# Optimization experiments

Measured on AMD Instinct MI355X. Metric: run time of the kernel, lower is better.

## Reference

```python
import jax, jax.numpy as jnp
import numpy as np
from jax import lax

B, T, H, F, K, NB, MAXLEN = 32, 1024, 384, 384, 3, 256, 2048


def _ln(x, g, b, eps=1e-5):
    m = jnp.mean(x, axis=-1, keepdims=True)
    v = jnp.var(x, axis=-1, keepdims=True)
    return (x - m) * lax.rsqrt(v + eps) * g + b


def _conv(x, w, b):
    # x: (B, T, Cin), w: (K, Cin, Cout); SAME padding == torch padding=(K-1)//2 for K=3, stride 1
    y = lax.conv_general_dilated(x, w, (1,), 'SAME', dimension_numbers=('NWC', 'WIO', 'NWC'))
    return y + b


def _predictor(x, mask, w1, b1, g1, be1, w2, b2, g2, be2, wo, bo):
    h = _ln(jax.nn.relu(_conv(x, w1, b1)), g1, be1)
    h = _ln(jax.nn.relu(_conv(h, w2, b2)), g2, be2)
    out = jnp.einsum('btf,f->bt', h, wo) + bo  # Linear(F -> 1).squeeze(-1)
    return jnp.where(mask, 0.0, out)


def _length_regulate(x, dur, max_len):
    # vectorized equivalent of torch per-sample expand+cat+pad
    csum = jnp.cumsum(dur, axis=1)                      # (B, T)
    total = csum[:, -1]                                 # (B,) = mel_len
    frames = jnp.arange(max_len)                        # (M,)
    # frame f belongs to phoneme i with csum[i-1] <= f < csum[i]
    idx = jax.vmap(lambda c: jnp.searchsorted(c, frames, side='right'))(csum)  # (B, M)
    idx = jnp.clip(idx, 0, x.shape[1] - 1)
    out = jnp.take_along_axis(x, idx[:, :, None], axis=1)                      # (B, M, H)
    valid = (frames[None, :] < total[:, None]).astype(x.dtype)                 # zero-pad tail
    return out * valid[:, :, None], total


def setup_inputs() -> dict:
    key = jax.random.key(0)
    ks = iter(jax.random.split(key, 64))
    nk = lambda: next(ks)
    d = {}
    d['x'] = jax.random.normal(nk(), (B, T, H), jnp.float32)
    d['src_mask'] = jnp.zeros((B, T), jnp.bool_)
    d['duration'] = jax.random.randint(nk(), (B, T), 0, 4)
    d['max_len'] = MAXLEN
    for p in ('dp', 'pp', 'ep'):
        d[p + '_w1'] = jax.random.normal(nk(), (K, H, F), jnp.float32) * 0.02
        d[p + '_b1'] = jnp.zeros((F,), jnp.float32)
        d[p + '_g1'] = jnp.ones((F,), jnp.float32)
        d[p + '_be1'] = jnp.zeros((F,), jnp.float32)
        d[p + '_w2'] = jax.random.normal(nk(), (K, F, F), jnp.float32) * 0.02
        d[p + '_b2'] = jnp.zeros((F,), jnp.float32)
        d[p + '_g2'] = jnp.ones((F,), jnp.float32)
        d[p + '_be2'] = jnp.zeros((F,), jnp.float32)
        d[p + '_wo'] = jax.random.normal(nk(), (F,), jnp.float32) * 0.02
        d[p + '_bo'] = jnp.zeros((1,), jnp.float32)
    d['pitch_bins'] = jnp.linspace(0.0, 1.0, NB - 1, dtype=jnp.float32)
    d['energy_bins'] = jnp.linspace(0.0, 1.0, NB - 1, dtype=jnp.float32)
    d['pitch_emb'] = jax.random.normal(nk(), (NB, H), jnp.float32) * 0.02
    d['energy_emb'] = jax.random.normal(nk(), (NB, H), jnp.float32) * 0.02
    d['pitch_target'] = jax.random.uniform(nk(), (B, T), jnp.float32)
    d['energy_target'] = jax.random.uniform(nk(), (B, T), jnp.float32)
    return d


def reference(x, src_mask, duration, max_len,
              dp_w1, dp_b1, dp_g1, dp_be1, dp_w2, dp_b2, dp_g2, dp_be2, dp_wo, dp_bo,
              pp_w1, pp_b1, pp_g1, pp_be1, pp_w2, pp_b2, pp_g2, pp_be2, pp_wo, pp_bo,
              ep_w1, ep_b1, ep_g1, ep_be1, ep_w2, ep_b2, ep_g2, ep_be2, ep_wo, ep_bo,
              pitch_bins, energy_bins, pitch_emb, energy_emb, pitch_target, energy_target):
    log_dur = _predictor(x, src_mask, dp_w1, dp_b1, dp_g1, dp_be1, dp_w2, dp_b2, dp_g2, dp_be2, dp_wo, dp_bo)
    # phoneme-level pitch (target path: bucketize target, torch.bucketize right=False == searchsorted left)
    pitch_pred = _predictor(x, src_mask, pp_w1, pp_b1, pp_g1, pp_be1, pp_w2, pp_b2, pp_g2, pp_be2, pp_wo, pp_bo)
    x = x + pitch_emb[jnp.searchsorted(pitch_bins, pitch_target, side='left')]
    # phoneme-level energy (predictor sees x AFTER pitch embedding add, as in torch)
    energy_pred = _predictor(x, src_mask, ep_w1, ep_b1, ep_g1, ep_be1, ep_w2, ep_b2, ep_g2, ep_be2, ep_wo, ep_bo)
    x = x + energy_emb[jnp.searchsorted(energy_bins, energy_target, side='left')]
    x_out, mel_len = _length_regulate(x, duration, max_len)
    return (x_out, pitch_pred, energy_pred, log_dur, mel_len)
```

## Files before the change

### kernel.cpp

```cpp
#include <hip/hip_runtime.h>

#define B_ 32
#define T_ 1024
#define C_ 384
#define MAXLEN_ 2048
#define NBINS_ 255
#define WPK1 442368
#define ARS 392
#define TROWS 62
#define NTILE 17

typedef __attribute__((ext_vector_type(8))) short short8v;
typedef __attribute__((ext_vector_type(4))) float floatx4;

__device__ __forceinline__ unsigned short f2bf(float f) {
    unsigned u = __float_as_uint(f);
    u += 0x7fffu + ((u >> 16) & 1u);
    return (unsigned short)(u >> 16);
}

__device__ __forceinline__ const unsigned short* rfl(const unsigned short* p) {
    unsigned long long u = (unsigned long long)p;
    unsigned lo = __builtin_amdgcn_readfirstlane((unsigned)u);
    unsigned hi = __builtin_amdgcn_readfirstlane((unsigned)(u >> 32));
    return (const unsigned short*)(((unsigned long long)hi << 32) | lo);
}

struct CvP {
    const float* xf;
    const unsigned short* wpk;
    const float* b1[3];  const float* g1[3];  const float* be1[3];
    const float* b2[3];  const float* g2[3];  const float* be2[3];
    const float* wo[3];  const float* bo[3];
    float* pred[3];
    const float* pbins; const float* pemb; const float* ptgt;
};

__global__ __launch_bounds__(512, 4) void conv_fused3(CvP P)
{
    __shared__ unsigned short As[66 * ARS];
    __shared__ float redS[8 * 64];
    __shared__ float redQ[8 * 64];
    __shared__ float prbuf[512];
    __shared__ int embi[66];

    const int tid  = threadIdx.x;
    const int wave = tid >> 6;
    const int lane = tid & 63;
    const int lq   = lane >> 4;
    const int ln   = lane & 15;
    const int blk  = blockIdx.x;
    const int p    = blk / (B_ * NTILE);
    const int rem  = blk - p * (B_ * NTILE);
    const int b    = rem / NTILE;
    const int k    = rem - b * NTILE;
    const int t0   = k * TROWS;
    const int nb   = wave * 48;

    const unsigned short* b1s = rfl(P.wpk + (size_t)p * WPK1 + wave * 1536);
    const int lo8 = lane * 8;
    short8v bA[3], bB[3];
#pragma unroll
    for (int nt = 0; nt < 3; ++nt) {
        bA[nt] = *(const short8v*)(b1s + lo8 + (nt << 9));
        bB[nt] = *(const short8v*)(b1s + lo8 + 12288 + (nt << 9));
    }

    const bool fuse_emb = (p == 2);
    if (fuse_emb) {
        if (tid < 66) {
            const int t = t0 - 2 + tid;
            int lo = 0;
            if ((unsigned)t < (unsigned)T_) {
                const float tg = P.ptgt[(b << 10) + t];
                int hi = NBINS_;
                while (lo < hi) {
                    const int mid = (lo + hi) >> 1;
                    if (P.pbins[mid] < tg) lo = mid + 1; else hi = mid;
                }
            }
            embi[tid] = lo;
        }
        __syncthreads();
    }
    for (int i = tid; i < 66 * 96; i += 512) {
        const int row = i / 96;
        const int c4  = i - row * 96;
        const int t   = t0 - 2 + row;
        uint2 pv = make_uint2(0u, 0u);
        if ((unsigned)t < (unsigned)T_) {
            float4 f = *(const float4*)(P.xf + ((size_t)(b << 10) + t) * C_ + c4 * 4);
            if (fuse_emb) {
                const float* er = P.pemb + (size_t)embi[row] * C_ + c4 * 4;
                f.x += er[0]; f.y += er[1]; f.z += er[2]; f.w += er[3];
            }
            asm("v_cvt_pk_bf16_f32 %0, %1, %2" : "=v"(pv.x) : "v"(f.x), "v"(f.y));
            asm("v_cvt_pk_bf16_f32 %0, %1, %2" : "=v"(pv.y) : "v"(f.z), "v"(f.w));
        }
        *(uint2*)&As[row * ARS + c4 * 4] = pv;
    }
    __syncthreads();

    floatx4 acc[12];
#pragma unroll
    for (int i = 0; i < 12; ++i) acc[i] = (floatx4){0.f, 0.f, 0.f, 0.f};

    const unsigned short* abase = &As[ln * ARS + lq * 8];

    {
        int offA = lo8 + 2 * 12288;
        int offB = lo8 + 3 * 12288;
#pragma unroll
        for (int kc = 0; kc < 3; ++kc) {
#pragma unroll
            for (int h2 = 0; h2 < 6; ++h2) {
                const int hb = h2 * 64;
                const int r  = kc * 12 + h2 * 2;
                {
                    short8v afrag[4];
#pragma unroll
                    for (int mt = 0; mt < 4; ++mt)
                        afrag[mt] = *(const short8v*)(abase + (mt * 16 + kc) * ARS + hb);
#pragma unroll
                    for (int mt = 0; mt < 4; ++mt)
#pragma unroll
                        for (int nt = 0; nt < 3; ++nt)
                            acc[mt * 3 + nt] = __builtin_amdgcn_mfma_f32_16x16x32_bf16(
                                afrag[mt], bA[nt], acc[mt * 3 + nt], 0, 0, 0);
                    if (r + 2 < 36) {
#pragma unroll
                        for (int nt = 0; nt < 3; ++nt)
                            bA[nt] = *(const short8v*)(b1s + offA + (nt << 9));
                        offA += 24576;
                    }
                }
                {
                    short8v afrag[4];
#pragma unroll
                    for (int mt = 0; mt < 4; ++mt)
                        afrag[mt] = *(const short8v*)(abase + (mt * 16 + kc) * ARS + hb + 32);
#pragma unroll
                    for (int mt = 0; mt < 4; ++mt)
#pragma unroll
                        for (int nt = 0; nt < 3; ++nt)
                            acc[mt * 3 + nt] = __builtin_amdgcn_mfma_f32_16x16x32_bf16(
                                afrag[mt], bB[nt], acc[mt * 3 + nt], 0, 0, 0);
                    if (r + 3 < 36) {
#pragma unroll
                        for (int nt = 0; nt < 3; ++nt)
                            bB[nt] = *(const short8v*)(b1s + offB + (nt << 9));
                        offB += 24576;
                    }
                }
            }
        }
    }
    __syncthreads();

    float c1b[3], c1g[3], c1be[3];
#pragma unroll
    for (int nt = 0; nt < 3; ++nt) {
        const int col = nb + nt * 16 + ln;
        c1b[nt]  = P.b1[p][col];
        c1g[nt]  = P.g1[p][col];
        c1be[nt] = P.be1[p][col];
    }
#pragma unroll
    for (int mt = 0; mt < 4; ++mt) {
#pragma unroll
        for (int rg = 0; rg < 4; ++rg) {
            float s = 0.f, q = 0.f;
#pragma unroll
            for (int nt = 0; nt < 3; ++nt) {
                float v = acc[mt * 3 + nt][rg] + c1b[nt];
                v = v > 0.f ? v : 0.f;
                acc[mt * 3 + nt][rg] = v;
                s += v; q += v * v;
            }
#pragma unroll
            for (int off = 1; off < 16; off <<= 1) {
                s += __shfl_xor(s, off, 64);
                q += __shfl_xor(q, off, 64);
            }
            if (ln == ((mt * 4 + rg) & 15)) {
                redS[wave * 64 + mt * 16 + lq * 4 + rg] = s;
                redQ[wave * 64 + mt * 16 + lq * 4 + rg] = q;
            }
        }
    }
    __syncthreads();

#pragma unroll
    for (int mt = 0; mt < 4; ++mt) {
#pragma unroll
        for (int rg = 0; rg < 4; ++rg) {
            const int j  = mt * 16 + lq * 4 + rg;
            const int th = t0 - 1 + j;
            float s = 0.f, q = 0.f;
#pragma unroll
            for (int w = 0; w < 8; ++w) {
                s += redS[w * 64 + j];
                q += redQ[w * 64 + j];
            }
            const float m  = s * (1.f / 384.f);
            const float rs = rsqrtf(q * (1.f / 384.f) - m * m + 1e-5f);
            const bool valid = (unsigned)th < (unsigned)T_;
#pragma unroll
            for (int nt = 0; nt < 3; ++nt) {
                float v = (acc[mt * 3 + nt][rg] - m) * rs * c1g[nt] + c1be[nt];
                if (!valid) v = 0.f;
                As[j * ARS + nb + nt * 16 + ln] = f2bf(v);
            }
        }
    }

    const unsigned short* b2s = rfl(P.wpk + (size_t)(3 + p) * WPK1 + wave * 1536);
#pragma unroll
    for (int nt = 0; nt < 3; ++nt) {
        bA[nt] = *(const short8v*)(b2s + lo8 + (nt << 9));
        bB[nt] = *(const short8v*)(b2s + lo8 + 12288 + (nt << 9));
    }
    __syncthreads();

#pragma unroll
    for (int i = 0; i < 12; ++i) acc[i] = (floatx4){0.f, 0.f, 0.f, 0.f};

    {
        int offA = lo8 + 2 * 12288;
        int offB = lo8 + 3 * 12288;
#pragma unroll
        for (int kc = 0; kc < 3; ++kc) {
#pragma unroll
            for (int h2 = 0; h2 < 6; ++h2) {
                const int hb = h2 * 64;
                const int r  = kc * 12 + h2 * 2;
                {
                    short8v afrag[4];
#pragma unroll
                    for (int mt = 0; mt < 4; ++mt)
                        afrag[mt] = *(const short8v*)(abase + (mt * 16 + kc) * ARS + hb);
#pragma unroll
                    for (int mt = 0; mt < 4; ++mt)
#pragma unroll
                        for (int nt = 0; nt < 3; ++nt)
                            acc[mt * 3 + nt] = __builtin_amdgcn_mfma_f32_16x16x32_bf16(
                                afrag[mt], bA[nt], acc[mt * 3 + nt], 0, 0, 0);
                    if (r + 2 < 36) {
#pragma unroll
                        for (int nt = 0; nt < 3; ++nt)
                            bA[nt] = *(const short8v*)(b2s + offA + (nt << 9));
                        offA += 24576;
                    }
                }
                {
                    short8v afrag[4];
#pragma unroll
                    for (int mt = 0; mt < 4; ++mt)
                        afrag[mt] = *(const short8v*)(abase + (mt * 16 + kc) * ARS + hb + 32);
#pragma unroll
                    for (int mt = 0; mt < 4; ++mt)
#pragma unroll
                        for (int nt = 0; nt < 3; ++nt)
                            acc[mt * 3 + nt] = __builtin_amdgcn_mfma_f32_16x16x32_bf16(
                                afrag[mt], bB[nt], acc[mt * 3 + nt], 0, 0, 0);
                    if (r + 3 < 36) {
#pragma unroll
                        for (int nt = 0; nt < 3; ++nt)
                            bB[nt] = *(const short8v*)(b2s + offB + (nt << 9));
                        offB += 24576;
                    }
                }
            }
        }
    }

    float c2b[3], c2g[3], c2be[3], cwo[3];
#pragma unroll
    for (int nt = 0; nt < 3; ++nt) {
        const int col = nb + nt * 16 + ln;
        c2b[nt]  = P.b2[p][col];
        c2g[nt]  = P.g2[p][col];
        c2be[nt] = P.be2[p][col];
        cwo[nt]  = P.wo[p][col];
    }
#pragma unroll
    for (int mt = 0; mt < 4; ++mt) {
#pragma unroll
        for (int rg = 0; rg < 4; ++rg) {
            float s = 0.f, q = 0.f;
#pragma unroll
            for (int nt = 0; nt < 3; ++nt) {
                float v = acc[mt * 3 + nt][rg] + c2b[nt];
                v = v > 0.f ? v : 0.f;
                acc[mt * 3 + nt][rg] = v;
                s += v; q += v * v;
            }
#pragma unroll
            for (int off = 1; off < 16; off <<= 1) {
                s += __shfl_xor(s, off, 64);
                q += __shfl_xor(q, off, 64);
            }
            if (ln == ((mt * 4 + rg) & 15)) {
                redS[wave * 64 + mt * 16 + lq * 4 + rg] = s;
                redQ[wave * 64 + mt * 16 + lq * 4 + rg] = q;
            }
        }
    }
    __syncthreads();

#pragma unroll
    for (int mt = 0; mt < 4; ++mt) {
#pragma unroll
        for (int rg = 0; rg < 4; ++rg) {
            const int row = mt * 16 + lq * 4 + rg;
            float s = 0.f, q = 0.f;
#pragma unroll
            for (int w = 0; w < 8; ++w) {
                s += redS[w * 64 + row];
                q += redQ[w * 64 + row];
            }
            const float m  = s * (1.f / 384.f);
            const float rs = rsqrtf(q * (1.f / 384.f) - m * m + 1e-5f);
            float pr = 0.f;
#pragma unroll
            for (int nt = 0; nt < 3; ++nt)
                pr += ((acc[mt * 3 + nt][rg] - m) * rs * c2g[nt] + c2be[nt]) * cwo[nt];
#pragma unroll
            for (int off = 1; off < 16; off <<= 1)
                pr += __shfl_xor(pr, off, 64);
            if (ln == ((mt * 4 + rg) & 15))
                prbuf[wave * 64 + row] = pr;
        }
    }
    __syncthreads();
    if (tid < 64) {
        const int t = t0 + tid;
        if (tid < TROWS && t < T_) {
            float s = P.bo[p][0];
#pragma unroll
            for (int w = 0; w < 8; ++w) s += prbuf[w * 64 + tid];
            P.pred[p][(b << 10) + t] = s;
        }
    }
}

#define WSS 388
__global__ __launch_bounds__(256) void pack_w_kernel(
    const float* __restrict__ s0, const float* __restrict__ s1,
    const float* __restrict__ s2, const float* __restrict__ s3,
    const float* __restrict__ s4, const float* __restrict__ s5,
    unsigned short* __restrict__ dst)
{
    __shared__ float ws[32 * WSS];
    const int blk  = blockIdx.x;
    const int wsel = blk / 36;
    const int r    = blk - wsel * 36;
    const float* src = wsel == 0 ? s0 : wsel == 1 ? s1 : wsel == 2 ? s2
                     : wsel == 3 ? s3 : wsel == 4 ? s4 : s5;
    const int tid = threadIdx.x;

    const float* sb = src + (size_t)r * 32 * C_;
    for (int i4 = tid; i4 < 3072; i4 += 256) {
        const int k  = i4 / 96;
        const int n4 = i4 - k * 96;
        *(float4*)&ws[k * WSS + n4 * 4] = *(const float4*)(sb + (size_t)k * C_ + n4 * 4);
    }
    __syncthreads();

    unsigned short* db = dst + (size_t)wsel * WPK1 + (size_t)r * 12288;
    for (int c = tid; c < 1536; c += 256) {
        const int lane = c & 63;
        const int wnt  = c >> 6;
        const int ln   = lane & 15;
        const int lq   = lane >> 4;
        const int n    = wnt * 16 + ln;
        ushort4 o0, o1;
        unsigned short e[8];
#pragma unroll
        for (int j = 0; j < 8; ++j)
            e[j] = f2bf(ws[(lq * 8 + j) * WSS + n]);
        o0 = make_ushort4(e[0], e[1], e[2], e[3]);
        o1 = make_ushort4(e[4], e[5], e[6], e[7]);
        *(ushort4*)(db + wnt * 512 + lane * 8)     = o0;
        *(ushort4*)(db + wnt * 512 + lane * 8 + 4) = o1;
    }
}

__global__ __launch_bounds__(256) void cumsum_idx_kernel(
    const int* __restrict__ dur,
    const float* __restrict__ pbins, const float* __restrict__ ptgt,
    const float* __restrict__ ebins, const float* __restrict__ etgt,
    int* __restrict__ xidx, float* __restrict__ mel_len)
{
    __shared__ int cs[T_];
    __shared__ int part[256];
    __shared__ float pb[NBINS_], eb[NBINS_];
    const int b = blockIdx.x;
    const int tid = threadIdx.x;
    if (tid < NBINS_) { pb[tid] = pbins[tid]; eb[tid] = ebins[tid]; }
    int l[4];
    int s = 0;
#pragma unroll
    for (int i = 0; i < 4; ++i) { l[i] = dur[(b << 10) + tid * 4 + i]; s += l[i]; }
    part[tid] = s;
    __syncthreads();
    for (int off = 1; off < 256; off <<= 1) {
        int u = 0;
        if (tid >= off) u = part[tid - off];
        __syncthreads();
        part[tid] += u;
        __syncthreads();
    }
    const int incl = part[tid];
    int run = incl - s;
#pragma unroll
    for (int i = 0; i < 4; ++i) {
        run += l[i];
        cs[tid * 4 + i] = run;
    }
    if (tid == 255) mel_len[b] = (float)incl;
    __syncthreads();
    const int total = cs[T_ - 1];
    for (int f = tid; f < MAXLEN_; f += 256) {
        int pk = -1;
        if (f < total) {
            int lo = 0, hi = T_;
            while (lo < hi) {
                const int mid = (lo + hi) >> 1;
                if (cs[mid] <= f) lo = mid + 1; else hi = mid;
            }
            const int t = lo > T_ - 1 ? T_ - 1 : lo;
            const int row = (b << 10) + t;
            const float ptg = ptgt[row];
            int plo = 0, phi = NBINS_;
            while (plo < phi) {
                const int mid = (plo + phi) >> 1;
                if (pb[mid] < ptg) plo = mid + 1; else phi = mid;
            }
            const float etg = etgt[row];
            int elo = 0, ehi = NBINS_;
            while (elo < ehi) {
                const int mid = (elo + ehi) >> 1;
                if (eb[mid] < etg) elo = mid + 1; else ehi = mid;
            }
            pk = t | (plo << 10) | (elo << 19);
        }
        xidx[(b << 11) + f] = pk;
    }
}

__global__ __launch_bounds__(256) void length_reg_kernel(
    const float* __restrict__ x, const int* __restrict__ xidx,
    const float* __restrict__ pemb, const float* __restrict__ eemb,
    float* __restrict__ out)
{
    const int g    = blockIdx.x * 256 + threadIdx.x;
    const int c4   = g % 96;
    const int rest = g / 96;
    const int frame = rest & (MAXLEN_ - 1);
    const int b     = rest >> 11;
    const int pk = xidx[(b << 11) + frame];
    float4 v = make_float4(0.f, 0.f, 0.f, 0.f);
    if (pk >= 0) {
        const int t   = pk & 1023;
        const int plo = (pk >> 10) & 511;
        const int elo = (pk >> 19) & 511;
        v = *(const float4*)(x + ((size_t)(b << 10) + t) * C_ + c4 * 4);
        const float4 pe = *(const float4*)(pemb + (size_t)plo * C_ + c4 * 4);
        const float4 ee = *(const float4*)(eemb + (size_t)elo * C_ + c4 * 4);
        v.x += pe.x + ee.x; v.y += pe.y + ee.y;
        v.z += pe.z + ee.z; v.w += pe.w + ee.w;
    }
    *(float4*)(out + (size_t)g * 4) = v;
}

extern "C" void kernel_launch(void* const* d_in, const int* in_sizes, int n_in,
                              void* d_out, int out_size, void* d_ws, size_t ws_size,
                              hipStream_t stream)
{
    const float* x        = (const float*)d_in[0];
    const int*   duration = (const int*)d_in[2];
    const float* P[3][10];
    for (int p = 0; p < 3; ++p)
        for (int q = 0; q < 10; ++q)
            P[p][q] = (const float*)d_in[4 + p * 10 + q];
    const float* pitch_bins    = (const float*)d_in[34];
    const float* energy_bins   = (const float*)d_in[35];
    const float* pitch_emb     = (const float*)d_in[36];
    const float* energy_emb    = (const float*)d_in[37];
    const float* pitch_target  = (const float*)d_in[38];
    const float* energy_target = (const float*)d_in[39];

    float* out_x      = (float*)d_out;
    float* out_pitch  = out_x + (size_t)B_ * MAXLEN_ * C_;
    float* out_energy = out_pitch + B_ * T_;
    float* out_logdur = out_energy + B_ * T_;
    float* out_mellen = out_logdur + B_ * T_;

    unsigned short* wpk = (unsigned short*)d_ws;
    int* xidx = (int*)(wpk + (size_t)6 * WPK1);

    const dim3 blk(256);
    const dim3 cblk(512);

    pack_w_kernel<<<216, blk, 0, stream>>>(
        P[0][0], P[0][4], P[1][0], P[1][4], P[2][0], P[2][4], wpk);

    CvP Pa;
    Pa.xf = x; Pa.wpk = wpk;
    for (int p = 0; p < 3; ++p) {
        Pa.b1[p]  = P[p][1];
        Pa.g1[p]  = P[p][2];
        Pa.be1[p] = P[p][3];
        Pa.b2[p]  = P[p][5];
        Pa.g2[p]  = P[p][6];
        Pa.be2[p] = P[p][7];
        Pa.wo[p]  = P[p][8];
        Pa.bo[p]  = P[p][9];
    }
    Pa.pred[0] = out_logdur; Pa.pred[1] = out_pitch; Pa.pred[2] = out_energy;
    Pa.pbins = pitch_bins; Pa.pemb = pitch_emb; Pa.ptgt = pitch_target;

    conv_fused3<<<3 * B_ * NTILE, cblk, 0, stream>>>(Pa);

    cumsum_idx_kernel<<<B_, blk, 0, stream>>>(
        duration, pitch_bins, pitch_target, energy_bins, energy_target,
        xidx, out_mellen);
    length_reg_kernel<<<24576, blk, 0, stream>>>(
        x, xidx, pitch_emb, energy_emb, out_x);
}
```

Before: 490.7 us.

## Add MFMA priority hints, centralize LayerNorm stats, restructure staging loop

Wraps each MFMA burst in s_setprio(1)/s_setprio(0) so waves issuing matrix ops get scheduling priority over waves doing loads. LayerNorm mean and rsqrt are now computed once per row by 64 threads into shared arrays, instead of every thread redundantly summing 8 partials per row. The input staging loop drops the per-iteration division for incremental row/column stepping. Gamma and beta loads are deferred to shorten register live ranges, at the cost of an extra barrier per LayerNorm.

```diff
diff --git a/kernel.cpp b/kernel.cpp
--- a/kernel.cpp
+++ b/kernel.cpp
@@ -42,6 +42,7 @@
     __shared__ float redS[8 * 64];
     __shared__ float redQ[8 * 64];
     __shared__ float prbuf[512];
+    __shared__ float mrsM[64], mrsR[64];
     __shared__ int embi[66];
 
     const int tid  = threadIdx.x;
@@ -83,21 +84,25 @@
         }
         __syncthreads();
     }
-    for (int i = tid; i < 66 * 96; i += 512) {
-        const int row = i / 96;
-        const int c4  = i - row * 96;
-        const int t   = t0 - 2 + row;
-        uint2 pv = make_uint2(0u, 0u);
-        if ((unsigned)t < (unsigned)T_) {
-            float4 f = *(const float4*)(P.xf + ((size_t)(b << 10) + t) * C_ + c4 * 4);
-            if (fuse_emb) {
-                const float* er = P.pemb + (size_t)embi[row] * C_ + c4 * 4;
-                f.x += er[0]; f.y += er[1]; f.z += er[2]; f.w += er[3];
-            }
-            asm("v_cvt_pk_bf16_f32 %0, %1, %2" : "=v"(pv.x) : "v"(f.x), "v"(f.y));
-            asm("v_cvt_pk_bf16_f32 %0, %1, %2" : "=v"(pv.y) : "v"(f.z), "v"(f.w));
-        }
-        *(uint2*)&As[row * ARS + c4 * 4] = pv;
+    {
+        int row = tid / 96;
+        int c4  = tid - row * 96;
+        while (row < 66) {
+            const int t = t0 - 2 + row;
+            uint2 pv = make_uint2(0u, 0u);
+            if ((unsigned)t < (unsigned)T_) {
+                float4 f = *(const float4*)(P.xf + ((size_t)(b << 10) + t) * C_ + c4 * 4);
+                if (fuse_emb) {
+                    const float* er = P.pemb + (size_t)embi[row] * C_ + c4 * 4;
+                    f.x += er[0]; f.y += er[1]; f.z += er[2]; f.w += er[3];
+                }
+                asm("v_cvt_pk_bf16_f32 %0, %1, %2" : "=v"(pv.x) : "v"(f.x), "v"(f.y));
+                asm("v_cvt_pk_bf16_f32 %0, %1, %2" : "=v"(pv.y) : "v"(f.z), "v"(f.w));
+            }
+            *(uint2*)&As[row * ARS + c4 * 4] = pv;
+            c4 += 32; row += 5;
+            if (c4 >= 96) { c4 -= 96; row += 1; }
+        }
     }
     __syncthreads();
 
@@ -121,12 +126,14 @@
 #pragma unroll
                     for (int mt = 0; mt < 4; ++mt)
                         afrag[mt] = *(const short8v*)(abase + (mt * 16 + kc) * ARS + hb);
+                    __builtin_amdgcn_s_setprio(1);
 #pragma unroll
                     for (int mt = 0; mt < 4; ++mt)
 #pragma unroll
                         for (int nt = 0; nt < 3; ++nt)
                             acc[mt * 3 + nt] = __builtin_amdgcn_mfma_f32_16x16x32_bf16(
                                 afrag[mt], bA[nt], acc[mt * 3 + nt], 0, 0, 0);
+                    __builtin_amdgcn_s_setprio(0);
                     if (r + 2 < 36) {
 #pragma unroll
                         for (int nt = 0; nt < 3; ++nt)
@@ -139,12 +146,14 @@
 #pragma unroll
                     for (int mt = 0; mt < 4; ++mt)
                         afrag[mt] = *(const short8v*)(abase + (mt * 16 + kc) * ARS + hb + 32);
+                    __builtin_amdgcn_s_setprio(1);
 #pragma unroll
                     for (int mt = 0; mt < 4; ++mt)
 #pragma unroll
                         for (int nt = 0; nt < 3; ++nt)
                             acc[mt * 3 + nt] = __builtin_amdgcn_mfma_f32_16x16x32_bf16(
                                 afrag[mt], bB[nt], acc[mt * 3 + nt], 0, 0, 0);
+                    __builtin_amdgcn_s_setprio(0);
                     if (r + 3 < 36) {
 #pragma unroll
                         for (int nt = 0; nt < 3; ++nt)
@@ -157,59 +166,72 @@
     }
     __syncthreads();
 
-    float c1b[3], c1g[3], c1be[3];
-#pragma unroll
-    for (int nt = 0; nt < 3; ++nt) {
-        const int col = nb + nt * 16 + ln;
-        c1b[nt]  = P.b1[p][col];
-        c1g[nt]  = P.g1[p][col];
-        c1be[nt] = P.be1[p][col];
-    }
-#pragma unroll
-    for (int mt = 0; mt < 4; ++mt) {
-#pragma unroll
-        for (int rg = 0; rg < 4; ++rg) {
-            float s = 0.f, q = 0.f;
-#pragma unroll
-            for (int nt = 0; nt < 3; ++nt) {
-                float v = acc[mt * 3 + nt][rg] + c1b[nt];
-                v = v > 0.f ? v : 0.f;
-                acc[mt * 3 + nt][rg] = v;
-                s += v; q += v * v;
-            }
-#pragma unroll
-            for (int off = 1; off < 16; off <<= 1) {
-                s += __shfl_xor(s, off, 64);
-                q += __shfl_xor(q, off, 64);
-            }
-            if (ln == ((mt * 4 + rg) & 15)) {
-                redS[wave * 64 + mt * 16 + lq * 4 + rg] = s;
-                redQ[wave * 64 + mt * 16 + lq * 4 + rg] = q;
-            }
-        }
-    }
-    __syncthreads();
-
-#pragma unroll
-    for (int mt = 0; mt < 4; ++mt) {
-#pragma unroll
-        for (int rg = 0; rg < 4; ++rg) {
-            const int j  = mt * 16 + lq * 4 + rg;
-            const int th = t0 - 1 + j;
-            float s = 0.f, q = 0.f;
-#pragma unroll
-            for (int w = 0; w < 8; ++w) {
-                s += redS[w * 64 + j];
-                q += redQ[w * 64 + j];
-            }
-            const float m  = s * (1.f / 384.f);
-            const float rs = rsqrtf(q * (1.f / 384.f) - m * m + 1e-5f);
-            const bool valid = (unsigned)th < (unsigned)T_;
-#pragma unroll
-            for (int nt = 0; nt < 3; ++nt) {
-                float v = (acc[mt * 3 + nt][rg] - m) * rs * c1g[nt] + c1be[nt];
-                if (!valid) v = 0.f;
-                As[j * ARS + nb + nt * 16 + ln] = f2bf(v);
+    {
+        float c1b[3];
+#pragma unroll
+        for (int nt = 0; nt < 3; ++nt)
+            c1b[nt] = P.b1[p][nb + nt * 16 + ln];
+#pragma unroll
+        for (int mt = 0; mt < 4; ++mt) {
+#pragma unroll
+            for (int rg = 0; rg < 4; ++rg) {
+                float s = 0.f, q = 0.f;
+#pragma unroll
+                for (int nt = 0; nt < 3; ++nt) {
+                    float v = acc[mt * 3 + nt][rg] + c1b[nt];
+                    v = v > 0.f ? v : 0.f;
+                    acc[mt * 3 + nt][rg] = v;
+                    s += v; q += v * v;
+                }
+#pragma unroll
+                for (int off = 1; off < 16; off <<= 1) {
+                    s += __shfl_xor(s, off, 64);
+                    q += __shfl_xor(q, off, 64);
+                }
+                if (ln == ((mt * 4 + rg) & 15)) {
+                    redS[wave * 64 + mt * 16 + lq * 4 + rg] = s;
+                    redQ[wave * 64 + mt * 16 + lq * 4 + rg] = q;
+                }
+            }
+        }
+    }
+    __syncthreads();
+
+    if (tid < 64) {
+        float s = 0.f, q = 0.f;
+#pragma unroll
+        for (int w = 0; w < 8; ++w) {
+            s += redS[w * 64 + tid];
+            q += redQ[w * 64 + tid];
+        }
+        const float m = s * (1.f / 384.f);
+        mrsM[tid] = m;
+        mrsR[tid] = rsqrtf(q * (1.f / 384.f) - m * m + 1e-5f);
+    }
+    __syncthreads();
+
+    {
+        float c1g[3], c1be[3];
+#pragma unroll
+        for (int nt = 0; nt < 3; ++nt) {
+            c1g[nt]  = P.g1[p][nb + nt * 16 + ln];
+            c1be[nt] = P.be1[p][nb + nt * 16 + ln];
+        }
+#pragma unroll
+        for (int mt = 0; mt < 4; ++mt) {
+#pragma unroll
+            for (int rg = 0; rg < 4; ++rg) {
+                const int j  = mt * 16 + lq * 4 + rg;
+                const int th = t0 - 1 + j;
+                const float m  = mrsM[j];
+                const float rs = mrsR[j];
+                const bool valid = (unsigned)th < (unsigned)T_;
+#pragma unroll
+                for (int nt = 0; nt < 3; ++nt) {
+                    float v = (acc[mt * 3 + nt][rg] - m) * rs * c1g[nt] + c1be[nt];
+                    if (!valid) v = 0.f;
+                    As[j * ARS + nb + nt * 16 + ln] = f2bf(v);
+                }
             }
         }
     }
@@ -239,12 +261,14 @@
 #pragma unroll
                     for (int mt = 0; mt < 4; ++mt)
                         afrag[mt] = *(const short8v*)(abase + (mt * 16 + kc) * ARS + hb);
+                    __builtin_amdgcn_s_setprio(1);
 #pragma unroll
                     for (int mt = 0; mt < 4; ++mt)
 #pragma unroll
                         for (int nt = 0; nt < 3; ++nt)
                             acc[mt * 3 + nt] = __builtin_amdgcn_mfma_f32_16x16x32_bf16(
                                 afrag[mt], bA[nt], acc[mt * 3 + nt], 0, 0, 0);
+                    __builtin_amdgcn_s_setprio(0);
                     if (r + 2 < 36) {
 #pragma unroll
                         for (int nt = 0; nt < 3; ++nt)
@@ -257,12 +281,14 @@
 #pragma unroll
                     for (int mt = 0; mt < 4; ++mt)
                         afrag[mt] = *(const short8v*)(abase + (mt * 16 + kc) * ARS + hb + 32);
+                    __builtin_amdgcn_s_setprio(1);
 #pragma unroll
                     for (int mt = 0; mt < 4; ++mt)
 #pragma unroll
                         for (int nt = 0; nt < 3; ++nt)
                             acc[mt * 3 + nt] = __builtin_amdgcn_mfma_f32_16x16x32_bf16(
                                 afrag[mt], bB[nt], acc[mt * 3 + nt], 0, 0, 0);
+                    __builtin_amdgcn_s_setprio(0);
                     if (r + 3 < 36) {
 #pragma unroll
                         for (int nt = 0; nt < 3; ++nt)
@@ -274,62 +300,75 @@
         }
     }
 
-    float c2b[3], c2g[3], c2be[3], cwo[3];
-#pragma unroll
-    for (int nt = 0; nt < 3; ++nt) {
-        const int col = nb + nt * 16 + ln;
-        c2b[nt]  = P.b2[p][col];
-        c2g[nt]  = P.g2[p][col];
-        c2be[nt] = P.be2[p][col];
-        cwo[nt]  = P.wo[p][col];
-    }
-#pragma unroll
-    for (int mt = 0; mt < 4; ++mt) {
-#pragma unroll
-        for (int rg = 0; rg < 4; ++rg) {
-            float s = 0.f, q = 0.f;
-#pragma unroll
-            for (int nt = 0; nt < 3; ++nt) {
-                float v = acc[mt * 3 + nt][rg] + c2b[nt];
-                v = v > 0.f ? v : 0.f;
-                acc[mt * 3 + nt][rg] = v;
-                s += v; q += v * v;
-            }
-#pragma unroll
-            for (int off = 1; off < 16; off <<= 1) {
-                s += __shfl_xor(s, off, 64);
-                q += __shfl_xor(q, off, 64);
-            }
-            if (ln == ((mt * 4 + rg) & 15)) {
-                redS[wave * 64 + mt * 16 + lq * 4 + rg] = s;
-                redQ[wave * 64 + mt * 16 + lq * 4 + rg] = q;
-            }
-        }
-    }
-    __syncthreads();
-
-#pragma unroll
-    for (int mt = 0; mt < 4; ++mt) {
-#pragma unroll
-        for (int rg = 0; rg < 4; ++rg) {
-            const int row = mt * 16 + lq * 4 + rg;
-            float s = 0.f, q = 0.f;
-#pragma unroll
-            for (int w = 0; w < 8; ++w) {
-                s += redS[w * 64 + row];
-                q += redQ[w * 64 + row];
-            }
-            const float m  = s * (1.f / 384.f);
-            const float rs = rsqrtf(q * (1.f / 384.f) - m * m + 1e-5f);
-            float pr = 0.f;
-#pragma unroll
-            for (int nt = 0; nt < 3; ++nt)
-                pr += ((acc[mt * 3 + nt][rg] - m) * rs * c2g[nt] + c2be[nt]) * cwo[nt];
-#pragma unroll
-            for (int off = 1; off < 16; off <<= 1)
-                pr += __shfl_xor(pr, off, 64);
-            if (ln == ((mt * 4 + rg) & 15))
-                prbuf[wave * 64 + row] = pr;
+    {
+        float c2b[3];
+#pragma unroll
+        for (int nt = 0; nt < 3; ++nt)
+            c2b[nt] = P.b2[p][nb + nt * 16 + ln];
+#pragma unroll
+        for (int mt = 0; mt < 4; ++mt) {
+#pragma unroll
+            for (int rg = 0; rg < 4; ++rg) {
+                float s = 0.f, q = 0.f;
+#pragma unroll
+                for (int nt = 0; nt < 3; ++nt) {
+                    float v = acc[mt * 3 + nt][rg] + c2b[nt];
+                    v = v > 0.f ? v : 0.f;
+                    acc[mt * 3 + nt][rg] = v;
+                    s += v; q += v * v;
+                }
+#pragma unroll
+                for (int off = 1; off < 16; off <<= 1) {
+                    s += __shfl_xor(s, off, 64);
+                    q += __shfl_xor(q, off, 64);
+                }
+                if (ln == ((mt * 4 + rg) & 15)) {
+                    redS[wave * 64 + mt * 16 + lq * 4 + rg] = s;
+                    redQ[wave * 64 + mt * 16 + lq * 4 + rg] = q;
+                }
+            }
+        }
+    }
+    __syncthreads();
+
+    if (tid < 64) {
+        float s = 0.f, q = 0.f;
+#pragma unroll
+        for (int w = 0; w < 8; ++w) {
+            s += redS[w * 64 + tid];
+            q += redQ[w * 64 + tid];
+        }
+        const float m = s * (1.f / 384.f);
+        mrsM[tid] = m;
+        mrsR[tid] = rsqrtf(q * (1.f / 384.f) - m * m + 1e-5f);
+    }
+    __syncthreads();
+
+    {
+        float c2g[3], c2be[3], cwo[3];
+#pragma unroll
+        for (int nt = 0; nt < 3; ++nt) {
+            c2g[nt]  = P.g2[p][nb + nt * 16 + ln];
+            c2be[nt] = P.be2[p][nb + nt * 16 + ln];
+            cwo[nt]  = P.wo[p][nb + nt * 16 + ln];
+        }
+#pragma unroll
+        for (int mt = 0; mt < 4; ++mt) {
+#pragma unroll
+            for (int rg = 0; rg < 4; ++rg) {
+                const int row = mt * 16 + lq * 4 + rg;
+                const float m  = mrsM[row];
+                const float rs = mrsR[row];
+                float pr = 0.f;
+#pragma unroll
+                for (int nt = 0; nt < 3; ++nt)
+                    pr += ((acc[mt * 3 + nt][rg] - m) * rs * c2g[nt] + c2be[nt]) * cwo[nt];
+#pragma unroll
+                for (int off = 1; off < 16; off <<= 1)
+                    pr += __shfl_xor(pr, off, 64);
+                if (ln == ((mt * 4 + rg) & 15))
+                    prbuf[wave * 64 + row] = pr;
+            }
         }
     }
     __syncthreads();
```

Result: faster. 442.7 us (-9.8%).
